# Performance work log

Measured on AMD Instinct MI355X. Metric: run time of the kernel, lower is better.

The kernel has to match this reference:

```python
import jax, jax.numpy as jnp
import numpy as np

# Dims: B nodes, Z species (elements), IN/OUT channels, M = 2*l+1 (l=1)
B, Z, IN, OUT, M = 8192, 10, 512, 512, 3
ALPHA = 1.0 / np.sqrt(IN)  # self.alpha = 1/sqrt(in_dim)
SQRT3 = float(np.sqrt(3.0))


def setup_inputs() -> dict:
    key = jax.random.key(0)
    k1, k2, k3 = jax.random.split(key, 3)
    t = jax.random.normal(k1, (B, IN, M), dtype=jnp.float32)
    species = jax.random.randint(k2, (B,), 0, Z)
    node_attrs = jax.nn.one_hot(species, Z, dtype=jnp.float32)  # [B, Z] one-hot
    # torch.nn.init.uniform_(weights, -sqrt(3), sqrt(3))
    weights = jax.random.uniform(k3, (Z, OUT, IN), dtype=jnp.float32,
                                 minval=-SQRT3, maxval=SQRT3)
    return {"t": t, "node_attrs": node_attrs, "weights": weights}


def reference(t, node_attrs, weights):
    # Faithful to: einsum('bz, zCc, bcd -> bCd', node_attrs, weights*alpha, t)
    # Contract weights with t first per species ([Z,B,C,M], ~500MB), which
    # avoids the huge [B,C,c] per-node weight-gather intermediate, then
    # select/sum over species with the one-hot node_attrs.
    W = weights * ALPHA                       # [Z, OUT, IN]
    zt = jnp.einsum('zCc,bcd->zbCd', W, t)    # [Z, B, OUT, M]
    out = jnp.einsum('bz,zbCd->bCd', node_attrs, zt)  # [B, OUT, M]
    return out
```

## Files before the change

### kernel.cpp

```cpp
#include <hip/hip_runtime.h>
#include <stdint.h>

#define NB   8192
#define NZ   10
#define CIN  512
#define COUT 512
#define MM   3
#define ALPHA 0.04419417382415922f

#define ROWS_TOTAL (NB * MM)
#define BM 128
#define BN 128
#define BK 32
#define KITERS (CIN / BK)
#define MAX_MT (ROWS_TOTAL / BM + NZ)
#define NGRP 32

typedef short bf16x8 __attribute__((ext_vector_type(8)));
typedef float f32x4  __attribute__((ext_vector_type(4)));

__device__ __forceinline__ uint16_t f2bf(float f) {
    union { float f; uint32_t i; } v; v.f = f;
    uint32_t x = v.i;
    x += 0x7fffu + ((x >> 16) & 1u);
    return (uint16_t)(x >> 16);
}
__device__ __forceinline__ uint32_t pack2(float a, float b) {
    return (uint32_t)f2bf(a) | ((uint32_t)f2bf(b) << 16);
}
__device__ __forceinline__ void async16(const ushort* g, ushort* l) {
    __builtin_amdgcn_global_load_lds((const uint32_t*)g, (uint32_t*)l, 16, 0, 0);
}

__global__ __launch_bounds__(256)
void prep_kernel(const float* __restrict__ attrs, const float* __restrict__ w,
                 int* __restrict__ species, int* __restrict__ hist,
                 ushort* __restrict__ wt) {
    const int tid = threadIdx.x;
    if (blockIdx.x >= NGRP) {
        const size_t i = ((size_t)(blockIdx.x - NGRP) * 256 + tid) * 8;
        float4 a = *(const float4*)(w + i);
        float4 b = *(const float4*)(w + i + 4);
        uint4 o;
        o.x = pack2(a.x, a.y); o.y = pack2(a.z, a.w);
        o.z = pack2(b.x, b.y); o.w = pack2(b.z, b.w);
        *(uint4*)(wt + i) = o;
        return;
    }
    __shared__ int wc[4][NZ];
    const int b = blockIdx.x * 256 + tid;
    const float* a = attrs + (size_t)b * NZ;
    int s = 0;
    #pragma unroll
    for (int z = 0; z < NZ; z++) if (a[z] > 0.5f) s = z;
    species[b] = s;
    const int wv = tid >> 6, lane = tid & 63;
    #pragma unroll
    for (int z = 0; z < NZ; z++) {
        unsigned long long m = __ballot(s == z);
        if (lane == 0) wc[wv][z] = __popcll(m);
    }
    __syncthreads();
    if (tid < NZ) {
        hist[blockIdx.x * NZ + tid] = wc[0][tid] + wc[1][tid] + wc[2][tid] + wc[3][tid];
    }
}

__global__ __launch_bounds__(256)
void place_kernel(const int* __restrict__ species, const int* __restrict__ hist,
                  int* __restrict__ sorted, int* __restrict__ offsets,
                  int* __restrict__ tile_offsets) {
    __shared__ int lhist[NGRP][NZ];
    __shared__ int loff[NZ + 1], ltoff[NZ + 1];
    __shared__ int pb[NZ];
    __shared__ int wc[4][NZ];
    const int tid = threadIdx.x, g = blockIdx.x;

    for (int i = tid; i < NGRP * NZ; i += 256) ((int*)lhist)[i] = hist[i];
    __syncthreads();
    if (tid == 0) {
        int off = 0, toff = 0;
        for (int z = 0; z < NZ; z++) {
            int tot = 0;
            for (int gg = 0; gg < NGRP; gg++) tot += lhist[gg][z];
            loff[z] = off; ltoff[z] = toff;
            off += tot;
            toff += (3 * tot + BM - 1) / BM;
        }
        loff[NZ] = off; ltoff[NZ] = toff;
    }
    __syncthreads();
    if (tid < NZ) {
        int base = loff[tid];
        for (int gg = 0; gg < g; gg++) base += lhist[gg][tid];
        pb[tid] = base;
    }
    if (g == 0 && tid < NZ + 1) {
        offsets[tid] = loff[tid];
        tile_offsets[tid] = ltoff[tid];
    }
    const int b = g * 256 + tid;
    const int s = species[b];
    const int wv = tid >> 6, lane = tid & 63;
    unsigned long long mymask = 0;
    #pragma unroll
    for (int z = 0; z < NZ; z++) {
        unsigned long long m = __ballot(s == z);
        if (lane == 0) wc[wv][z] = __popcll(m);
        if (s == z) mymask = m;
    }
    __syncthreads();
    int rank = __popcll(mymask & ((1ull << lane) - 1ull));
    #pragma unroll
    for (int w2 = 0; w2 < 4; w2++) if (w2 < wv) rank += wc[w2][s];
    sorted[pb[s] + rank] = b;
}

__global__ __launch_bounds__(256)
void pack_t(const float* __restrict__ t, const int* __restrict__ sorted,
            ushort* __restrict__ tt) {
    const int w = threadIdx.x >> 6, L = threadIdx.x & 63;
    const int p = blockIdx.x * 4 + w;
    const int node = sorted[p];
    const float4* src = (const float4*)(t + (size_t)node * (CIN * MM) + L * 24);
    float4 f[6];
    #pragma unroll
    for (int i = 0; i < 6; i++) f[i] = src[i];
    const float* v = (const float*)f;
    #pragma unroll
    for (int d = 0; d < MM; d++) {
        uint4 o;
        o.x = pack2(v[d],      v[3 + d]);
        o.y = pack2(v[6 + d],  v[9 + d]);
        o.z = pack2(v[12 + d], v[15 + d]);
        o.w = pack2(v[18 + d], v[21 + d]);
        *(uint4*)&tt[(size_t)(3 * p + d) * CIN + L * 8] = o;
    }
}

__global__ __launch_bounds__(256)
void gemm_kernel(const ushort* __restrict__ tt, const ushort* __restrict__ wt,
                 const int* __restrict__ sorted, const int* __restrict__ offsets,
                 const int* __restrict__ tile_offsets, float* __restrict__ out) {
    __shared__ ushort As[BM][BK];
    __shared__ ushort Bs[BN][BK];
    __shared__ int spos[48];

    const int tz = blockIdx.x;
    if (tz >= tile_offsets[NZ]) return;
    int z = 0;
    #pragma unroll
    for (int i = 1; i < NZ; i++) if (tile_offsets[i] <= tz) z = i;

    const int row_base = 3 * offsets[z] + (tz - tile_offsets[z]) * BM;
    const int row_end  = 3 * offsets[z + 1];
    const int pos0     = row_base / 3;
    const int Cbase    = blockIdx.y * BN;

    const int tid = threadIdx.x;
    const int w = tid >> 6, L = tid & 63;

    if (tid < 48) spos[tid] = sorted[min(pos0 + tid, NB - 1)];

    const int lrow = L >> 2;
    const int lk   = (L & 3) * 8;
    const ushort* gA = tt + (size_t)(row_base + w * 32 + lrow) * CIN + lk;
    const ushort* gB = wt + ((size_t)z * COUT + Cbase + w * 32 + lrow) * CIN + lk;
    ushort* lA0 = &As[w * 32][0];
    ushort* lA1 = &As[w * 32 + 16][0];
    ushort* lB0 = &Bs[w * 32][0];
    ushort* lB1 = &Bs[w * 32 + 16][0];

    const int wm = w & 1, wn = w >> 1;
    const int q = L >> 4, mr = L & 15;

    f32x4 acc[4][4];
    #pragma unroll
    for (int i = 0; i < 4; i++)
        #pragma unroll
        for (int j = 0; j < 4; j++) acc[i][j] = (f32x4){0.f, 0.f, 0.f, 0.f};

    for (int kt = 0; kt < KITERS; kt++) {
        const int ko = kt * BK;
        async16(gA + ko, lA0);
        async16(gA + (size_t)16 * CIN + ko, lA1);
        async16(gB + ko, lB0);
        async16(gB + (size_t)16 * CIN + ko, lB1);
        __syncthreads();

        bf16x8 af[4], bf[4];
        #pragma unroll
        for (int am = 0; am < 4; am++)
            af[am] = *(const bf16x8*)&As[wm * 64 + am * 16 + mr][q * 8];
        #pragma unroll
        for (int bn = 0; bn < 4; bn++)
            bf[bn] = *(const bf16x8*)&Bs[wn * 64 + bn * 16 + mr][q * 8];
        #pragma unroll
        for (int am = 0; am < 4; am++)
            #pragma unroll
            for (int bn = 0; bn < 4; bn++)
                acc[am][bn] = __builtin_amdgcn_mfma_f32_16x16x32_bf16(
                    af[am], bf[bn], acc[am][bn], 0, 0, 0);
        __syncthreads();
    }

    #pragma unroll
    for (int am = 0; am < 4; am++) {
        #pragma unroll
        for (int r = 0; r < 4; r++) {
            const int Rg = row_base + wm * 64 + am * 16 + q * 4 + r;
            if (Rg < row_end) {
                const int pos = Rg / 3;
                const int d = Rg - 3 * pos;
                const int node = spos[pos - pos0];
                float* o = out + (size_t)node * (COUT * MM) + d;
                #pragma unroll
                for (int bn = 0; bn < 4; bn++) {
                    const int Cg = Cbase + wn * 64 + bn * 16 + mr;
                    o[(size_t)Cg * 3] = ALPHA * acc[am][bn][r];
                }
            }
        }
    }
}

extern "C" void kernel_launch(void* const* d_in, const int* in_sizes, int n_in,
                              void* d_out, int out_size, void* d_ws, size_t ws_size,
                              hipStream_t stream) {
    const float* t     = (const float*)d_in[0];
    const float* attrs = (const float*)d_in[1];
    const float* w     = (const float*)d_in[2];
    float* out = (float*)d_out;

    uint8_t* ws = (uint8_t*)d_ws;
    int* species      = (int*)ws;                  ws += NB * 4;
    int* sorted       = (int*)ws;                  ws += NB * 4;
    int* hist         = (int*)ws;                  ws += NGRP * NZ * 4;
    int* offsets      = (int*)ws;                  ws += 16 * 4;
    int* tile_offsets = (int*)ws;                  ws += 16 * 4;
    ws = (uint8_t*)(((uintptr_t)ws + 255) & ~(uintptr_t)255);
    ushort* wt = (ushort*)ws;                      ws += (size_t)NZ * COUT * CIN * 2;
    ushort* tt = (ushort*)ws;

    hipLaunchKernelGGL(prep_kernel, dim3(NGRP + (NZ * COUT * CIN) / 2048), dim3(256),
                       0, stream, attrs, w, species, hist, wt);
    hipLaunchKernelGGL(place_kernel, dim3(NGRP), dim3(256), 0, stream,
                       species, hist, sorted, offsets, tile_offsets);
    hipLaunchKernelGGL(pack_t, dim3(NB / 4), dim3(256), 0, stream, t, sorted, tt);
    hipLaunchKernelGGL(gemm_kernel, dim3(MAX_MT, COUT / BN), dim3(256), 0, stream,
                       tt, wt, sorted, offsets, tile_offsets, out);
}
```

Before: 153.8 us.

## Double-buffer LDS tiles with k-chunk-major layout to overlap loads and MFMA

Splits the LDS A/B tiles into two buffers and prefetches the next K slice with async global-to-LDS copies while MFMAs run on the current one, removing one barrier per iteration. The LDS layout becomes k-chunk-major so each wave loads 64 consecutive rows of one 8-element chunk and fragment reads are contiguous, reducing bank conflicts. LDS usage doubles, and correctness relies on the end-of-iteration barrier draining outstanding async loads.

```diff
diff --git a/kernel.cpp b/kernel.cpp
--- a/kernel.cpp
+++ b/kernel.cpp
@@ -142,8 +142,8 @@
 void gemm_kernel(const ushort* __restrict__ tt, const ushort* __restrict__ wt,
                  const int* __restrict__ sorted, const int* __restrict__ offsets,
                  const int* __restrict__ tile_offsets, float* __restrict__ out) {
-    __shared__ ushort As[BM][BK];
-    __shared__ ushort Bs[BN][BK];
+    __shared__ ushort As[2][BK / 8][BM][8];
+    __shared__ ushort Bs[2][BK / 8][BN][8];
     __shared__ int spos[48];
 
     const int tz = blockIdx.x;
@@ -162,14 +162,10 @@
 
     if (tid < 48) spos[tid] = sorted[min(pos0 + tid, NB - 1)];
 
-    const int lrow = L >> 2;
-    const int lk   = (L & 3) * 8;
-    const ushort* gA = tt + (size_t)(row_base + w * 32 + lrow) * CIN + lk;
-    const ushort* gB = wt + ((size_t)z * COUT + Cbase + w * 32 + lrow) * CIN + lk;
-    ushort* lA0 = &As[w * 32][0];
-    ushort* lA1 = &As[w * 32 + 16][0];
-    ushort* lB0 = &Bs[w * 32][0];
-    ushort* lB1 = &Bs[w * 32 + 16][0];
+    const ushort* gA0 = tt + (size_t)(row_base + L) * CIN + w * 8;
+    const ushort* gA1 = gA0 + (size_t)64 * CIN;
+    const ushort* gB0 = wt + ((size_t)z * COUT + Cbase + L) * CIN + w * 8;
+    const ushort* gB1 = gB0 + (size_t)64 * CIN;
 
     const int wm = w & 1, wn = w >> 1;
     const int q = L >> 4, mr = L & 15;
@@ -180,29 +176,37 @@
         #pragma unroll
         for (int j = 0; j < 4; j++) acc[i][j] = (f32x4){0.f, 0.f, 0.f, 0.f};
 
+#define STAGE(bufi, ko) do {                       \
+        async16(gA0 + (ko), &As[bufi][w][0][0]);   \
+        async16(gA1 + (ko), &As[bufi][w][64][0]);  \
+        async16(gB0 + (ko), &Bs[bufi][w][0][0]);   \
+        async16(gB1 + (ko), &Bs[bufi][w][64][0]);  \
+    } while (0)
+
+    STAGE(0, 0);
+    __syncthreads();
+
     for (int kt = 0; kt < KITERS; kt++) {
-        const int ko = kt * BK;
-        async16(gA + ko, lA0);
-        async16(gA + (size_t)16 * CIN + ko, lA1);
-        async16(gB + ko, lB0);
-        async16(gB + (size_t)16 * CIN + ko, lB1);
-        __syncthreads();
+        const int cur = kt & 1;
+        if (kt + 1 < KITERS) STAGE(cur ^ 1, (kt + 1) * BK);
 
         bf16x8 af[4], bf[4];
         #pragma unroll
         for (int am = 0; am < 4; am++)
-            af[am] = *(const bf16x8*)&As[wm * 64 + am * 16 + mr][q * 8];
+            af[am] = *(const bf16x8*)&As[cur][q][wm * 64 + am * 16 + mr][0];
         #pragma unroll
         for (int bn = 0; bn < 4; bn++)
-            bf[bn] = *(const bf16x8*)&Bs[wn * 64 + bn * 16 + mr][q * 8];
+            bf[bn] = *(const bf16x8*)&Bs[cur][q][wn * 64 + bn * 16 + mr][0];
         #pragma unroll
         for (int am = 0; am < 4; am++)
             #pragma unroll
             for (int bn = 0; bn < 4; bn++)
                 acc[am][bn] = __builtin_amdgcn_mfma_f32_16x16x32_bf16(
                     af[am], bf[bn], acc[am][bn], 0, 0, 0);
+
         __syncthreads();
     }
+#undef STAGE
 
     #pragma unroll
     for (int am = 0; am < 4; am++) {
```

After: 159.7 us. +3.8%, slower.
